# Kernel tuning notes

Hardware: AMD Instinct MI355X
Metric: run time of the kernel (lower is better)

Reference implementation:

```python
import jax, jax.numpy as jnp
import numpy as np

N_ATOMS = 512
N_MOL = 16
HIDDEN = 128
FILTERS = 128
NUM_RBF = 50
CUTOFF = 10.0
N_LAYERS = 3


def setup_inputs() -> dict:
    key = jax.random.key(0)
    ks = jax.random.split(key, 20)
    s = 0.05
    inp = {
        "atomic_numbers": jax.random.randint(ks[0], (N_ATOMS,), 0, 100),
        "positions": jax.random.uniform(ks[1], (N_ATOMS, 3), jnp.float32) * CUTOFF,
        "batch": jnp.sort(jax.random.randint(ks[2], (N_ATOMS,), 0, N_MOL)),
        # parameters (linear weights stored as [in, out])
        "emb": jax.random.normal(ks[3], (100, HIDDEN), jnp.float32) * s,
        "fw1": jax.random.normal(ks[4], (N_LAYERS, NUM_RBF, FILTERS), jnp.float32) * s,
        "fb1": jnp.zeros((N_LAYERS, FILTERS), jnp.float32),
        "fw2": jax.random.normal(ks[5], (N_LAYERS, FILTERS, FILTERS), jnp.float32) * s,
        "fb2": jnp.zeros((N_LAYERS, FILTERS), jnp.float32),
        "d1w": jax.random.normal(ks[6], (N_LAYERS, HIDDEN, FILTERS), jnp.float32) * s,
        "d1b": jnp.zeros((N_LAYERS, FILTERS), jnp.float32),
        "d2w": jax.random.normal(ks[7], (N_LAYERS, FILTERS, HIDDEN), jnp.float32) * s,
        "d2b": jnp.zeros((N_LAYERS, HIDDEN), jnp.float32),
        "ow1": jax.random.normal(ks[8], (HIDDEN, HIDDEN // 2), jnp.float32) * s,
        "ob1": jnp.zeros((HIDDEN // 2,), jnp.float32),
        "ow2": jax.random.normal(ks[9], (HIDDEN // 2, 1), jnp.float32) * s,
        "ob2": jnp.zeros((1,), jnp.float32),
    }
    return inp


def _schnet_fwd(atomic_numbers, positions, batch, emb, fw1, fb1, fw2, fb2,
                d1w, d1b, d2w, d2b, ow1, ob1, ow2, ob2):
    N = positions.shape[0]
    x = emb[atomic_numbers]                                  # [N, H]

    # all-pairs distances (safe sqrt for the zero diagonal)
    diff = positions[:, None, :] - positions[None, :, :]     # [N, N, 3]
    d2 = jnp.sum(diff * diff, axis=-1)                       # [N, N]
    d = jnp.sqrt(jnp.where(d2 > 0, d2, 1.0))
    d = jnp.where(d2 > 0, d, 0.0)

    eye = jnp.eye(N, dtype=bool)
    valid = (~eye) & (d < CUTOFF)                            # no self-edges, within cutoff

    # gaussian RBF embedding of distances
    centers = jnp.linspace(0.0, CUTOFF, NUM_RBF)             # [R]
    width = CUTOFF / NUM_RBF
    rbf = jnp.exp(-((d[..., None] - centers) ** 2) / (2.0 * width * width))  # [N, N, R]

    # cosine cutoff envelope; zero on invalid edges -> messages identical to edge-list version
    env = 0.5 * (jnp.cos(d * jnp.pi / CUTOFF) + 1.0) * valid.astype(d.dtype)  # [N, N]

    for l in range(N_LAYERS):
        filt = jax.nn.silu(rbf @ fw1[l] + fb1[l]) @ fw2[l] + fb2[l]   # [N, N, F]
        filt = filt * env[..., None]
        xj = x @ d1w[l] + d1b[l]                                      # [N, F] source features
        # message[i,j] = xj[i] * filt[i,j]; scatter-add to destination j
        agg = jnp.einsum('if,ijf->jf', xj, filt)                      # [N, F]
        x = x + agg @ d2w[l] + d2b[l]

    # mean-pool atoms per molecule
    mol_sum = jax.ops.segment_sum(x, batch, num_segments=N_MOL)       # [M, H]
    counts = jax.ops.segment_sum(jnp.ones((N,), x.dtype), batch, num_segments=N_MOL)
    mol = mol_sum / jnp.clip(counts, 1.0)[:, None]

    h = jax.nn.silu(mol @ ow1 + ob1)
    return h @ ow2 + ob2                                              # [M, 1]


def reference(atomic_numbers, positions, batch, emb, fw1, fb1, fw2, fb2,
              d1w, d1b, d2w, d2b, ow1, ob1, ow2, ob2):
    return _schnet_fwd(atomic_numbers, positions, batch, emb, fw1, fb1, fw2, fb2,
                       d1w, d1b, d2w, d2b, ow1, ob1, ow2, ob2)
```

## Files before the change

kernel.cpp:

```cpp
#include <hip/hip_runtime.h>
#include <math.h>

#define N_ATOMS 512
#define N_MOL   16
#define HIDDEN  128
#define FILTERS 128
#define NUM_RBF 50
#define CUTOFF  10.0f
#define N_LAYERS 3

#define KBINS  1024
#define PROWS  (KBINS + 1)
#define TB     32
#define TBLK   33
#define EMB_BLOCKS 16

__device__ __forceinline__ unsigned short f2bf(float v) {
    unsigned u = __float_as_uint(v);
    u += 0x7fffu + ((u >> 16) & 1u);
    return (unsigned short)(u >> 16);
}
__device__ __forceinline__ float bf2f(unsigned short u) {
    return __uint_as_float((unsigned)u << 16);
}

__global__ void __launch_bounds__(256) k_front(
        const int* __restrict__ an, const float* __restrict__ emb,
        const float* __restrict__ d1w, const float* __restrict__ d1b,
        const float* __restrict__ fw1, const float* __restrict__ fb1,
        const float* __restrict__ fw2, const float* __restrict__ fb2,
        float* __restrict__ x, unsigned short* __restrict__ xj,
        unsigned short* __restrict__ tab) {
    __shared__ __align__(16) float s_h[TB][132];
    __shared__ float s_rbf[TB][50];
    __shared__ int   s_an[32];
    int bid = blockIdx.x, t = threadIdx.x;
    int cq = t & 31, bg = t >> 5;

    if (bid < EMB_BLOCKS) {
        int i0 = bid * 32;
        if (t < 32) s_an[t] = an[i0 + t];
        __syncthreads();
        for (int idx = t; idx < 32 * HIDDEN; idx += 256) {
            int a = idx >> 7, c = idx & 127;
            float v = emb[(size_t)s_an[a] * HIDDEN + c];
            s_h[a][c] = v;
            x[(size_t)(i0 + a) * HIDDEN + c] = v;
        }
        __syncthreads();
        float o[4][4];
        float4 bv = *(const float4*)(d1b + 4 * cq);
        float bva[4] = { bv.x, bv.y, bv.z, bv.w };
        #pragma unroll
        for (int aa = 0; aa < 4; aa++)
            #pragma unroll
            for (int cc = 0; cc < 4; cc++) o[aa][cc] = bva[cc];
        #pragma unroll 4
        for (int h = 0; h < HIDDEN; h += 2) {
            float4 wA = *(const float4*)(d1w + (size_t)h * FILTERS + 4 * cq);
            float4 wB = *(const float4*)(d1w + (size_t)(h + 1) * FILTERS + 4 * cq);
            float wa[4] = { wA.x, wA.y, wA.z, wA.w };
            float wb[4] = { wB.x, wB.y, wB.z, wB.w };
            #pragma unroll
            for (int aa = 0; aa < 4; aa++) {
                float2 hp = *(const float2*)(&s_h[4 * bg + aa][h]);
                #pragma unroll
                for (int cc = 0; cc < 4; cc++) {
                    o[aa][cc] = fmaf(hp.x, wa[cc], o[aa][cc]);
                    o[aa][cc] = fmaf(hp.y, wb[cc], o[aa][cc]);
                }
            }
        }
        #pragma unroll
        for (int aa = 0; aa < 4; aa++) {
            int i = i0 + 4 * bg + aa;
            #pragma unroll
            for (int cp = 0; cp < 2; cp++) {
                unsigned int pk = (unsigned)f2bf(o[aa][2 * cp]) |
                                  ((unsigned)f2bf(o[aa][2 * cp + 1]) << 16);
                *(unsigned int*)(xj + (size_t)i * FILTERS + 4 * cq + 2 * cp) = pk;
            }
        }
    } else {
        int tb = bid - EMB_BLOCKS;
        int l  = tb / TBLK, bx = tb % TBLK;
        int bin0 = bx * TB;
        const float* w1g = fw1 + (size_t)l * NUM_RBF * FILTERS;
        const float* w2g = fw2 + (size_t)l * FILTERS * FILTERS;
        for (int idx = t; idx < TB * NUM_RBF; idx += 256) {
            int b = idx / NUM_RBF, r = idx - b * NUM_RBF;
            float dd = (bin0 + b) * (CUTOFF / (float)KBINS);
            float cr = r * (CUTOFF / (float)(NUM_RBF - 1));
            float xx = dd - cr;
            s_rbf[b][r] = expf(-xx * xx * 12.5f);
        }
        __syncthreads();
        float hreg[4][4];
        float4 b1v = *(const float4*)(fb1 + (size_t)l * FILTERS + 4 * cq);
        float b1a[4] = { b1v.x, b1v.y, b1v.z, b1v.w };
        #pragma unroll
        for (int bb = 0; bb < 4; bb++)
            #pragma unroll
            for (int cc = 0; cc < 4; cc++) hreg[bb][cc] = b1a[cc];
        #pragma unroll 2
        for (int r = 0; r < NUM_RBF; r++) {
            float4 w = *(const float4*)(w1g + (size_t)r * FILTERS + 4 * cq);
            float wa[4] = { w.x, w.y, w.z, w.w };
            #pragma unroll
            for (int bb = 0; bb < 4; bb++) {
                float rb = s_rbf[4 * bg + bb][r];
                #pragma unroll
                for (int cc = 0; cc < 4; cc++) hreg[bb][cc] = fmaf(rb, wa[cc], hreg[bb][cc]);
            }
        }
        #pragma unroll
        for (int bb = 0; bb < 4; bb++) {
            float4 sv;
            sv.x = hreg[bb][0] / (1.f + expf(-hreg[bb][0]));
            sv.y = hreg[bb][1] / (1.f + expf(-hreg[bb][1]));
            sv.z = hreg[bb][2] / (1.f + expf(-hreg[bb][2]));
            sv.w = hreg[bb][3] / (1.f + expf(-hreg[bb][3]));
            *(float4*)(&s_h[4 * bg + bb][4 * cq]) = sv;
        }
        __syncthreads();
        float o[4][4];
        float4 b2v = *(const float4*)(fb2 + (size_t)l * FILTERS + 4 * cq);
        float b2a[4] = { b2v.x, b2v.y, b2v.z, b2v.w };
        #pragma unroll
        for (int bb = 0; bb < 4; bb++)
            #pragma unroll
            for (int cc = 0; cc < 4; cc++) o[bb][cc] = b2a[cc];
        #pragma unroll 4
        for (int hh = 0; hh < FILTERS; hh += 2) {
            float4 wA = *(const float4*)(w2g + (size_t)hh * FILTERS + 4 * cq);
            float4 wB = *(const float4*)(w2g + (size_t)(hh + 1) * FILTERS + 4 * cq);
            float wa[4] = { wA.x, wA.y, wA.z, wA.w };
            float wb[4] = { wB.x, wB.y, wB.z, wB.w };
            #pragma unroll
            for (int bb = 0; bb < 4; bb++) {
                float2 hp = *(const float2*)(&s_h[4 * bg + bb][hh]);
                #pragma unroll
                for (int cc = 0; cc < 4; cc++) {
                    o[bb][cc] = fmaf(hp.x, wa[cc], o[bb][cc]);
                    o[bb][cc] = fmaf(hp.y, wb[cc], o[bb][cc]);
                }
            }
        }
        size_t base = (size_t)l * PROWS * FILTERS * 2;
        #pragma unroll
        for (int bb = 0; bb < 4; bb++) {
            int bin = bin0 + 4 * bg + bb;
            float dd = bin * (CUTOFF / (float)KBINS);
            float env = (bin >= KBINS) ? 0.f
                      : 0.5f * (cosf(dd * (3.14159265358979f / CUTOFF)) + 1.f);
            #pragma unroll
            for (int cc = 0; cc < 4; cc++) {
                int c = 4 * cq + cc;
                unsigned short pb = f2bf(o[bb][cc] * env);
                if (bin <= KBINS)                 tab[base + ((size_t)bin * FILTERS + c) * 2 + 0] = pb;
                if (bin >= 1 && bin <= KBINS + 1) tab[base + ((size_t)(bin - 1) * FILTERS + c) * 2 + 1] = pb;
            }
        }
    }
}

template<int FIRST, int LAST>
__global__ void __launch_bounds__(512) k_layer(const float* __restrict__ pos,
        float2* __restrict__ kw, const unsigned int* __restrict__ tab,
        const unsigned short* __restrict__ xj_in, float* __restrict__ x,
        const float* __restrict__ w2, const float* __restrict__ b2,
        const float* __restrict__ w1n, const float* __restrict__ b1n,
        unsigned short* __restrict__ xj_out) {
    int j = blockIdx.x;
    int t = threadIdx.x, f = t & 127, q = t >> 7;
    __shared__ float2 s_kw[N_ATOMS];
    __shared__ float  s_red[4][FILTERS];
    __shared__ float  s_agg[FILTERS];
    __shared__ float  s_xn[HIDDEN];
    __shared__ float  s_pos[FIRST ? N_ATOMS * 3 : 1];
    if (FIRST) {
        for (int idx = t; idx < N_ATOMS * 3; idx += 512) s_pos[idx] = pos[idx];
        __syncthreads();
        float pjx = s_pos[j*3+0], pjy = s_pos[j*3+1], pjz = s_pos[j*3+2];
        float dx = s_pos[t*3+0] - pjx;
        float dy = s_pos[t*3+1] - pjy;
        float dz = s_pos[t*3+2] - pjz;
        float d  = sqrtf(dx*dx + dy*dy + dz*dz);
        int   k; float w;
        if (t == j || d >= CUTOFF) { k = KBINS; w = 0.f; }
        else {
            float tt = d * ((float)KBINS / CUTOFF);
            k = (int)tt;
            if (k > KBINS - 1) k = KBINS - 1;
            w = tt - (float)k;
        }
        float2 kv = make_float2(w, __int_as_float(k));
        s_kw[t] = kv;
        kw[(size_t)j * N_ATOMS + t] = kv;
        __syncthreads();
    } else {
        s_kw[t] = kw[(size_t)j * N_ATOMS + t];
        __syncthreads();
    }
    float acc0 = 0.f, acc1 = 0.f, acc2 = 0.f, acc3 = 0.f;
    int i0 = q * 128;
    #pragma unroll 2
    for (int ii = 0; ii < 128; ii += 4) {
        float2 kv0 = s_kw[i0 + ii];
        float2 kv1 = s_kw[i0 + ii + 1];
        float2 kv2 = s_kw[i0 + ii + 2];
        float2 kv3 = s_kw[i0 + ii + 3];
        unsigned int p0 = tab[(size_t)__float_as_int(kv0.y) * FILTERS + f];
        unsigned int p1 = tab[(size_t)__float_as_int(kv1.y) * FILTERS + f];
        unsigned int p2 = tab[(size_t)__float_as_int(kv2.y) * FILTERS + f];
        unsigned int p3 = tab[(size_t)__float_as_int(kv3.y) * FILTERS + f];
        float xv0 = bf2f(xj_in[(size_t)(i0 + ii    ) * FILTERS + f]);
        float xv1 = bf2f(xj_in[(size_t)(i0 + ii + 1) * FILTERS + f]);
        float xv2 = bf2f(xj_in[(size_t)(i0 + ii + 2) * FILTERS + f]);
        float xv3 = bf2f(xj_in[(size_t)(i0 + ii + 3) * FILTERS + f]);
        float lo0 = __uint_as_float(p0 << 16), hi0 = __uint_as_float(p0 & 0xffff0000u);
        float lo1 = __uint_as_float(p1 << 16), hi1 = __uint_as_float(p1 & 0xffff0000u);
        float lo2 = __uint_as_float(p2 << 16), hi2 = __uint_as_float(p2 & 0xffff0000u);
        float lo3 = __uint_as_float(p3 << 16), hi3 = __uint_as_float(p3 & 0xffff0000u);
        acc0 = fmaf(xv0, fmaf(kv0.x, hi0 - lo0, lo0), acc0);
        acc1 = fmaf(xv1, fmaf(kv1.x, hi1 - lo1, lo1), acc1);
        acc2 = fmaf(xv2, fmaf(kv2.x, hi2 - lo2, lo2), acc2);
        acc3 = fmaf(xv3, fmaf(kv3.x, hi3 - lo3, lo3), acc3);
    }
    s_red[q][f] = (acc0 + acc1) + (acc2 + acc3);
    __syncthreads();
    if (q == 0) s_agg[f] = s_red[0][f] + s_red[1][f] + s_red[2][f] + s_red[3][f];
    __syncthreads();
    float v = 0.f;
    int ff0 = q * 32;
    #pragma unroll 8
    for (int ff = ff0; ff < ff0 + 32; ff++) v = fmaf(s_agg[ff], w2[ff*HIDDEN + f], v);
    s_red[q][f] = v;
    __syncthreads();
    if (q == 0) {
        float xnew = x[j*HIDDEN + f] + b2[f] + s_red[0][f] + s_red[1][f] + s_red[2][f] + s_red[3][f];
        x[j*HIDDEN + f] = xnew;
        s_xn[f] = xnew;
    }
    __syncthreads();
    if (!LAST) {
        float a2 = 0.f;
        int h0 = q * 32;
        #pragma unroll 8
        for (int hh = h0; hh < h0 + 32; hh++) a2 = fmaf(s_xn[hh], w1n[hh*FILTERS + f], a2);
        s_red[q][f] = a2;
        __syncthreads();
        if (q == 0) xj_out[(size_t)j*FILTERS + f] =
            f2bf(b1n[f] + s_red[0][f] + s_red[1][f] + s_red[2][f] + s_red[3][f]);
    }
}

__device__ __forceinline__ int lbound(const int* __restrict__ b, int n, int v) {
    int lo = 0, hi = n;
    while (lo < hi) { int mid = (lo + hi) >> 1; if (b[mid] < v) lo = mid + 1; else hi = mid; }
    return lo;
}

__global__ void __launch_bounds__(128) k_pool(const float* __restrict__ x,
        const int* __restrict__ batch, const float* __restrict__ ow1,
        const float* __restrict__ ob1, const float* __restrict__ ow2,
        const float* __restrict__ ob2, float* __restrict__ out) {
    int m = blockIdx.x, t = threadIdx.x;
    int lo = lbound(batch, N_ATOMS, m);
    int hi = lbound(batch, N_ATOMS, m + 1);
    float s = 0.f;
    for (int i = lo; i < hi; i++) s += x[i*HIDDEN + t];
    int cnt = hi - lo;
    float mol = s / (float)(cnt > 0 ? cnt : 1);
    __shared__ float s_mol[HIDDEN];
    __shared__ float s_h[HIDDEN/2];
    s_mol[t] = mol;
    __syncthreads();
    if (t < HIDDEN/2) {
        float a = ob1[t];
        for (int h = 0; h < HIDDEN; h++) a = fmaf(s_mol[h], ow1[h*(HIDDEN/2) + t], a);
        s_h[t] = a / (1.f + expf(-a));
    }
    __syncthreads();
    if (t == 0) {
        float a = ob2[0];
        for (int h = 0; h < HIDDEN/2; h++) a = fmaf(s_h[h], ow2[h], a);
        out[m] = a;
    }
}

extern "C" void kernel_launch(void* const* d_in, const int* in_sizes, int n_in,
                              void* d_out, int out_size, void* d_ws, size_t ws_size,
                              hipStream_t stream) {
    const int*   an    = (const int*)  d_in[0];
    const float* pos   = (const float*)d_in[1];
    const int*   batch = (const int*)  d_in[2];
    const float* emb   = (const float*)d_in[3];
    const float* fw1   = (const float*)d_in[4];
    const float* fb1   = (const float*)d_in[5];
    const float* fw2   = (const float*)d_in[6];
    const float* fb2   = (const float*)d_in[7];
    const float* d1w   = (const float*)d_in[8];
    const float* d1b   = (const float*)d_in[9];
    const float* d2w   = (const float*)d_in[10];
    const float* d2b   = (const float*)d_in[11];
    const float* ow1   = (const float*)d_in[12];
    const float* ob1   = (const float*)d_in[13];
    const float* ow2   = (const float*)d_in[14];
    const float* ob2   = (const float*)d_in[15];
    float* out = (float*)d_out;

    float*          ws   = (float*)d_ws;
    float2*         kw   = (float2*)ws;
    float*          x    = (float*)(kw + (size_t)N_ATOMS * N_ATOMS);
    unsigned short* xjA  = (unsigned short*)(x + N_ATOMS * HIDDEN);
    unsigned short* xjB  = xjA + (size_t)N_ATOMS * FILTERS;
    unsigned short* tab  = xjB + (size_t)N_ATOMS * FILTERS;

    k_front<<<EMB_BLOCKS + N_LAYERS * TBLK, 256, 0, stream>>>(
        an, emb, d1w, d1b, fw1, fb1, fw2, fb2, x, xjA, tab);

    const unsigned int* t0 = (const unsigned int*)(tab + (size_t)0 * PROWS * FILTERS * 2);
    const unsigned int* t1 = (const unsigned int*)(tab + (size_t)1 * PROWS * FILTERS * 2);
    const unsigned int* t2 = (const unsigned int*)(tab + (size_t)2 * PROWS * FILTERS * 2);

    k_layer<1,0><<<N_ATOMS, 512, 0, stream>>>(pos, kw, t0, xjA, x,
        d2w + (size_t)0*FILTERS*HIDDEN, d2b + (size_t)0*HIDDEN,
        d1w + (size_t)1*HIDDEN*FILTERS, d1b + (size_t)1*FILTERS, xjB);
    k_layer<0,0><<<N_ATOMS, 512, 0, stream>>>(pos, kw, t1, xjB, x,
        d2w + (size_t)1*FILTERS*HIDDEN, d2b + (size_t)1*HIDDEN,
        d1w + (size_t)2*HIDDEN*FILTERS, d1b + (size_t)2*FILTERS, xjA);
    k_layer<0,1><<<N_ATOMS, 512, 0, stream>>>(pos, kw, t2, xjA, x,
        d2w + (size_t)2*FILTERS*HIDDEN, d2b + (size_t)2*HIDDEN,
        d1w, d1b, xjB);

    k_pool<<<N_MOL, 128, 0, stream>>>(x, batch, ow1, ob1, ow2, ob2, out);
}
```

Measured before the change: 73.58 us.

## Spread filter-table build over one wavefront per bin and parallelize pooling

The filter-table part of the front kernel changes from 32-bin register tiles in 99 blocks to one 64-lane wavefront per bin, giving about 385 blocks of 512 threads. RBF values are computed inline with fast exp and cos intrinsics. The embedding/xj projection now uses 8 blocks of 64 atoms. The pooling kernel replaces two serial binary searches with a parallel count using shared atomics, splits the atom sum across two halves, splits the MLP reduction across threads, and ends with a wavefront shuffle reduction. The aim is more parallelism in the small front and tail kernels, at the cost of less register reuse of the weights per thread and slightly lower precision from the fast intrinsics.

```diff
diff --git a/kernel.cpp b/kernel.cpp
--- a/kernel.cpp
+++ b/kernel.cpp
@@ -10,10 +10,12 @@
 #define N_LAYERS 3
 
 #define KBINS  1024
+#define NBINS  (KBINS + 2)
 #define PROWS  (KBINS + 1)
-#define TB     32
-#define TBLK   33
-#define EMB_BLOCKS 16
+#define TOTW   (N_LAYERS * NBINS)
+#define TWBLK  ((TOTW + 7) / 8)
+#define EMBB   8
+#define PI_F   3.14159265358979f
 
 __device__ __forceinline__ unsigned short f2bf(float v) {
     unsigned u = __float_as_uint(v);
@@ -24,30 +26,76 @@
     return __uint_as_float((unsigned)u << 16);
 }
 
-__global__ void __launch_bounds__(256) k_front(
+__global__ void __launch_bounds__(512) k_front(
         const int* __restrict__ an, const float* __restrict__ emb,
         const float* __restrict__ d1w, const float* __restrict__ d1b,
         const float* __restrict__ fw1, const float* __restrict__ fb1,
         const float* __restrict__ fw2, const float* __restrict__ fb2,
         float* __restrict__ x, unsigned short* __restrict__ xj,
         unsigned short* __restrict__ tab) {
-    __shared__ __align__(16) float s_h[TB][132];
-    __shared__ float s_rbf[TB][50];
-    __shared__ int   s_an[32];
+    __shared__ float s_sh[8][HIDDEN];
+    __shared__ __align__(16) float s_row[64][HIDDEN];
+    __shared__ int   s_an[64];
     int bid = blockIdx.x, t = threadIdx.x;
-    int cq = t & 31, bg = t >> 5;
-
-    if (bid < EMB_BLOCKS) {
-        int i0 = bid * 32;
-        if (t < 32) s_an[t] = an[i0 + t];
-        __syncthreads();
-        for (int idx = t; idx < 32 * HIDDEN; idx += 256) {
+
+    if (bid < TWBLK) {
+        int wv = t >> 6, lane = t & 63;
+        int w  = bid * 8 + wv;
+        int wc = w < TOTW ? w : TOTW - 1;
+        int l  = wc / NBINS;
+        int bin = wc - l * NBINS;
+        float dd = bin * (CUTOFF / (float)KBINS);
+        const float* w1g = fw1 + (size_t)l * NUM_RBF * FILTERS;
+        const float* w2g = fw2 + (size_t)l * FILTERS * FILTERS;
+        int c0 = lane, c1 = lane + 64;
+        float h0 = fb1[l * FILTERS + c0];
+        float h1 = fb1[l * FILTERS + c1];
+        #pragma unroll 5
+        for (int r = 0; r < NUM_RBF; r++) {
+            float cr = r * (CUTOFF / (float)(NUM_RBF - 1));
+            float xx = dd - cr;
+            float rb = __expf(-xx * xx * 12.5f);
+            h0 = fmaf(rb, w1g[r * FILTERS + c0], h0);
+            h1 = fmaf(rb, w1g[r * FILTERS + c1], h1);
+        }
+        s_sh[wv][c0] = h0 / (1.f + __expf(-h0));
+        s_sh[wv][c1] = h1 / (1.f + __expf(-h1));
+        __syncthreads();
+        float o0 = fb2[l * FILTERS + c0];
+        float o1 = fb2[l * FILTERS + c1];
+        #pragma unroll 4
+        for (int hh = 0; hh < FILTERS; hh++) {
+            float hv = s_sh[wv][hh];
+            o0 = fmaf(hv, w2g[hh * FILTERS + c0], o0);
+            o1 = fmaf(hv, w2g[hh * FILTERS + c1], o1);
+        }
+        float env = (bin >= KBINS) ? 0.f
+                  : 0.5f * (__cosf(dd * (PI_F / CUTOFF)) + 1.f);
+        unsigned short p0 = f2bf(o0 * env), p1 = f2bf(o1 * env);
+        size_t base = (size_t)l * PROWS * FILTERS * 2;
+        if (w < TOTW) {
+            if (bin <= KBINS) {
+                tab[base + ((size_t)bin * FILTERS + c0) * 2 + 0] = p0;
+                tab[base + ((size_t)bin * FILTERS + c1) * 2 + 0] = p1;
+            }
+            if (bin >= 1) {
+                tab[base + ((size_t)(bin - 1) * FILTERS + c0) * 2 + 1] = p0;
+                tab[base + ((size_t)(bin - 1) * FILTERS + c1) * 2 + 1] = p1;
+            }
+        }
+    } else {
+        int eb = bid - TWBLK;
+        int i0 = eb * 64;
+        if (t < 64) s_an[t] = an[i0 + t];
+        __syncthreads();
+        for (int idx = t; idx < 64 * HIDDEN; idx += 512) {
             int a = idx >> 7, c = idx & 127;
             float v = emb[(size_t)s_an[a] * HIDDEN + c];
-            s_h[a][c] = v;
+            s_row[a][c] = v;
             x[(size_t)(i0 + a) * HIDDEN + c] = v;
         }
         __syncthreads();
+        int cq = t & 31, ag = t >> 5;
         float o[4][4];
         float4 bv = *(const float4*)(d1b + 4 * cq);
         float bva[4] = { bv.x, bv.y, bv.z, bv.w };
@@ -63,7 +111,7 @@
             float wb[4] = { wB.x, wB.y, wB.z, wB.w };
             #pragma unroll
             for (int aa = 0; aa < 4; aa++) {
-                float2 hp = *(const float2*)(&s_h[4 * bg + aa][h]);
+                float2 hp = *(const float2*)(&s_row[ag * 4 + aa][h]);
                 #pragma unroll
                 for (int cc = 0; cc < 4; cc++) {
                     o[aa][cc] = fmaf(hp.x, wa[cc], o[aa][cc]);
@@ -73,92 +121,12 @@
         }
         #pragma unroll
         for (int aa = 0; aa < 4; aa++) {
-            int i = i0 + 4 * bg + aa;
+            int i = i0 + ag * 4 + aa;
             #pragma unroll
             for (int cp = 0; cp < 2; cp++) {
                 unsigned int pk = (unsigned)f2bf(o[aa][2 * cp]) |
                                   ((unsigned)f2bf(o[aa][2 * cp + 1]) << 16);
                 *(unsigned int*)(xj + (size_t)i * FILTERS + 4 * cq + 2 * cp) = pk;
-            }
-        }
-    } else {
-        int tb = bid - EMB_BLOCKS;
-        int l  = tb / TBLK, bx = tb % TBLK;
-        int bin0 = bx * TB;
-        const float* w1g = fw1 + (size_t)l * NUM_RBF * FILTERS;
-        const float* w2g = fw2 + (size_t)l * FILTERS * FILTERS;
-        for (int idx = t; idx < TB * NUM_RBF; idx += 256) {
-            int b = idx / NUM_RBF, r = idx - b * NUM_RBF;
-            float dd = (bin0 + b) * (CUTOFF / (float)KBINS);
-            float cr = r * (CUTOFF / (float)(NUM_RBF - 1));
-            float xx = dd - cr;
-            s_rbf[b][r] = expf(-xx * xx * 12.5f);
-        }
-        __syncthreads();
-        float hreg[4][4];
-        float4 b1v = *(const float4*)(fb1 + (size_t)l * FILTERS + 4 * cq);
-        float b1a[4] = { b1v.x, b1v.y, b1v.z, b1v.w };
-        #pragma unroll
-        for (int bb = 0; bb < 4; bb++)
-            #pragma unroll
-            for (int cc = 0; cc < 4; cc++) hreg[bb][cc] = b1a[cc];
-        #pragma unroll 2
-        for (int r = 0; r < NUM_RBF; r++) {
-            float4 w = *(const float4*)(w1g + (size_t)r * FILTERS + 4 * cq);
-            float wa[4] = { w.x, w.y, w.z, w.w };
-            #pragma unroll
-            for (int bb = 0; bb < 4; bb++) {
-                float rb = s_rbf[4 * bg + bb][r];
-                #pragma unroll
-                for (int cc = 0; cc < 4; cc++) hreg[bb][cc] = fmaf(rb, wa[cc], hreg[bb][cc]);
-            }
-        }
-        #pragma unroll
-        for (int bb = 0; bb < 4; bb++) {
-            float4 sv;
-            sv.x = hreg[bb][0] / (1.f + expf(-hreg[bb][0]));
-            sv.y = hreg[bb][1] / (1.f + expf(-hreg[bb][1]));
-            sv.z = hreg[bb][2] / (1.f + expf(-hreg[bb][2]));
-            sv.w = hreg[bb][3] / (1.f + expf(-hreg[bb][3]));
-            *(float4*)(&s_h[4 * bg + bb][4 * cq]) = sv;
-        }
-        __syncthreads();
-        float o[4][4];
-        float4 b2v = *(const float4*)(fb2 + (size_t)l * FILTERS + 4 * cq);
-        float b2a[4] = { b2v.x, b2v.y, b2v.z, b2v.w };
-        #pragma unroll
-        for (int bb = 0; bb < 4; bb++)
-            #pragma unroll
-            for (int cc = 0; cc < 4; cc++) o[bb][cc] = b2a[cc];
-        #pragma unroll 4
-        for (int hh = 0; hh < FILTERS; hh += 2) {
-            float4 wA = *(const float4*)(w2g + (size_t)hh * FILTERS + 4 * cq);
-            float4 wB = *(const float4*)(w2g + (size_t)(hh + 1) * FILTERS + 4 * cq);
-            float wa[4] = { wA.x, wA.y, wA.z, wA.w };
-            float wb[4] = { wB.x, wB.y, wB.z, wB.w };
-            #pragma unroll
-            for (int bb = 0; bb < 4; bb++) {
-                float2 hp = *(const float2*)(&s_h[4 * bg + bb][hh]);
-                #pragma unroll
-                for (int cc = 0; cc < 4; cc++) {
-                    o[bb][cc] = fmaf(hp.x, wa[cc], o[bb][cc]);
-                    o[bb][cc] = fmaf(hp.y, wb[cc], o[bb][cc]);
-                }
-            }
-        }
-        size_t base = (size_t)l * PROWS * FILTERS * 2;
-        #pragma unroll
-        for (int bb = 0; bb < 4; bb++) {
-            int bin = bin0 + 4 * bg + bb;
-            float dd = bin * (CUTOFF / (float)KBINS);
-            float env = (bin >= KBINS) ? 0.f
-                      : 0.5f * (cosf(dd * (3.14159265358979f / CUTOFF)) + 1.f);
-            #pragma unroll
-            for (int cc = 0; cc < 4; cc++) {
-                int c = 4 * cq + cc;
-                unsigned short pb = f2bf(o[bb][cc] * env);
-                if (bin <= KBINS)                 tab[base + ((size_t)bin * FILTERS + c) * 2 + 0] = pb;
-                if (bin >= 1 && bin <= KBINS + 1) tab[base + ((size_t)(bin - 1) * FILTERS + c) * 2 + 1] = pb;
             }
         }
     }
@@ -255,37 +223,50 @@
     }
 }
 
-__device__ __forceinline__ int lbound(const int* __restrict__ b, int n, int v) {
-    int lo = 0, hi = n;
-    while (lo < hi) { int mid = (lo + hi) >> 1; if (b[mid] < v) lo = mid + 1; else hi = mid; }
-    return lo;
-}
-
-__global__ void __launch_bounds__(128) k_pool(const float* __restrict__ x,
+__global__ void __launch_bounds__(256) k_pool(const float* __restrict__ x,
         const int* __restrict__ batch, const float* __restrict__ ow1,
         const float* __restrict__ ob1, const float* __restrict__ ow2,
         const float* __restrict__ ob2, float* __restrict__ out) {
     int m = blockIdx.x, t = threadIdx.x;
-    int lo = lbound(batch, N_ATOMS, m);
-    int hi = lbound(batch, N_ATOMS, m + 1);
+    __shared__ float s_red[2][FILTERS];
+    __shared__ float s_mol[HIDDEN];
+    __shared__ float s_hh[64];
+    __shared__ int   s_lo, s_cnt;
+    if (t == 0) { s_lo = 0; s_cnt = 0; }
+    __syncthreads();
+    {
+        int b0 = batch[t], b1 = batch[t + 256];
+        int mylo  = (b0 <  m) + (b1 <  m);
+        int mycnt = (b0 == m) + (b1 == m);
+        atomicAdd(&s_lo, mylo);
+        atomicAdd(&s_cnt, mycnt);
+    }
+    __syncthreads();
+    int lo = s_lo, cnt = s_cnt, hi = lo + cnt;
+    int f = t & 127, half = t >> 7;
     float s = 0.f;
-    for (int i = lo; i < hi; i++) s += x[i*HIDDEN + t];
-    int cnt = hi - lo;
-    float mol = s / (float)(cnt > 0 ? cnt : 1);
-    __shared__ float s_mol[HIDDEN];
-    __shared__ float s_h[HIDDEN/2];
-    s_mol[t] = mol;
-    __syncthreads();
-    if (t < HIDDEN/2) {
-        float a = ob1[t];
-        for (int h = 0; h < HIDDEN; h++) a = fmaf(s_mol[h], ow1[h*(HIDDEN/2) + t], a);
-        s_h[t] = a / (1.f + expf(-a));
-    }
-    __syncthreads();
-    if (t == 0) {
-        float a = ob2[0];
-        for (int h = 0; h < HIDDEN/2; h++) a = fmaf(s_h[h], ow2[h], a);
-        out[m] = a;
+    for (int i = lo + half; i < hi; i += 2) s += x[(size_t)i * HIDDEN + f];
+    s_red[half][f] = s;
+    __syncthreads();
+    if (half == 0) s_mol[f] = (s_red[0][f] + s_red[1][f]) / (float)(cnt > 0 ? cnt : 1);
+    __syncthreads();
+    int o = t & 63, sl = t >> 6;
+    float a = 0.f;
+    #pragma unroll 8
+    for (int h = sl * 32; h < sl * 32 + 32; h++) a = fmaf(s_mol[h], ow1[h * 64 + o], a);
+    float* sr = (float*)s_red;
+    __syncthreads();
+    sr[sl * 64 + o] = a;
+    __syncthreads();
+    if (t < 64) {
+        float v = ob1[t] + sr[t] + sr[64 + t] + sr[128 + t] + sr[192 + t];
+        s_hh[t] = v / (1.f + __expf(-v));
+    }
+    __syncthreads();
+    if (t < 64) {
+        float v = s_hh[t] * ow2[t];
+        for (int off = 32; off > 0; off >>= 1) v += __shfl_down(v, off, 64);
+        if (t == 0) out[m] = v + ob2[0];
     }
 }
 
@@ -317,7 +298,7 @@
     unsigned short* xjB  = xjA + (size_t)N_ATOMS * FILTERS;
     unsigned short* tab  = xjB + (size_t)N_ATOMS * FILTERS;
 
-    k_front<<<EMB_BLOCKS + N_LAYERS * TBLK, 256, 0, stream>>>(
+    k_front<<<TWBLK + EMBB, 512, 0, stream>>>(
         an, emb, d1w, d1b, fw1, fb1, fw2, fb2, x, xjA, tab);
 
     const unsigned int* t0 = (const unsigned int*)(tab + (size_t)0 * PROWS * FILTERS * 2);
@@ -334,5 +315,5 @@
         d2w + (size_t)2*FILTERS*HIDDEN, d2b + (size_t)2*HIDDEN,
         d1w, d1b, xjB);
 
-    k_pool<<<N_MOL, 128, 0, stream>>>(x, batch, ow1, ob1, ow2, ob2, out);
-}
+    k_pool<<<N_MOL, 256, 0, stream>>>(x, batch, ow1, ob1, ow2, ob2, out);
+}
```

After: 74.46 us. Within noise of the previous version (+1.2%).
